# Optimization experiments

Hardware: AMD Instinct MI355X
Metric: run time of the kernel (lower is better)

## Reference

```python
import jax, jax.numpy as jnp
import numpy as np

D = 1024
H = 16
EPS = 1e-5


def setup_inputs() -> dict:
    key = jax.random.key(0)
    ks = jax.random.split(key, 6)
    B, T, d = 4, 2048, D
    s = 0.02
    return {
        "x": jax.random.normal(ks[0], (B, T, d), jnp.float32),
        "w_attn": jax.random.normal(ks[1], (d, 3 * d), jnp.float32) * s,
        "w_o": jax.random.normal(ks[2], (d, d), jnp.float32) * s,
        "ln1_g": jnp.ones((d,), jnp.float32),
        "ln1_b": jnp.zeros((d,), jnp.float32),
        "ln2_g": jnp.ones((d,), jnp.float32),
        "ln2_b": jnp.zeros((d,), jnp.float32),
        "w_fc": jax.random.normal(ks[3], (d, 4 * d), jnp.float32) * s,
        "b_fc": jnp.zeros((4 * d,), jnp.float32),
        "w_proj": jax.random.normal(ks[4], (4 * d, d), jnp.float32) * s,
        "b_proj": jnp.zeros((d,), jnp.float32),
    }


def _layernorm(x, g, b):
    mu = jnp.mean(x, axis=-1, keepdims=True)
    var = jnp.mean(jnp.square(x - mu), axis=-1, keepdims=True)
    return (x - mu) * jax.lax.rsqrt(var + EPS) * g + b


def _attention(x, w_attn, w_o):
    B, T, d = x.shape
    hd = d // H
    qkv = x @ w_attn  # [B,T,3d]
    q, k, v = jnp.split(qkv, 3, axis=-1)
    q = q.reshape(B, T, H, hd).transpose(0, 2, 1, 3)  # [B,H,T,hd]
    k = k.reshape(B, T, H, hd).transpose(0, 2, 1, 3)
    v = v.reshape(B, T, H, hd).transpose(0, 2, 1, 3)
    att = jnp.einsum("bhqd,bhkd->bhqk", q, k) * (1.0 / np.sqrt(hd))
    mask = jnp.tril(jnp.ones((T, T), bool))
    att = jnp.where(mask, att, jnp.float32(-jnp.inf))
    att = jax.nn.softmax(att, axis=-1)
    y = jnp.einsum("bhqk,bhkd->bhqd", att, v)
    y = y.transpose(0, 2, 1, 3).reshape(B, T, d)
    return y @ w_o


def reference(x, w_attn, w_o, ln1_g, ln1_b, ln2_g, ln2_b, w_fc, b_fc, w_proj, b_proj):
    x = x + _attention(_layernorm(x, ln1_g, ln1_b), w_attn, w_o)
    h = _layernorm(x, ln2_g, ln2_b)
    h = jax.nn.gelu(h @ w_fc + b_fc, approximate=True)
    return x + h @ w_proj + b_proj
```

## Files before the change

### kernel.cpp

```cpp
#include <hip/hip_runtime.h>
#include <math.h>

#define D_MODEL 1024
#define NHEAD   16
#define HDIM    64
#define SEQ     2048
#define BATCH   4
#define NROWS   (BATCH*SEQ)

using bf16x8 = __attribute__((ext_vector_type(8))) short;
using bf16x4 = __attribute__((ext_vector_type(4))) short;
using f32x4  = __attribute__((ext_vector_type(4))) float;

__device__ __forceinline__ unsigned short f2bf(float f) {
    unsigned u = __float_as_uint(f);
    u += 0x7fffu + ((u >> 16) & 1u);
    return (unsigned short)(u >> 16);
}
__device__ __forceinline__ float bf2f(unsigned short h) {
    unsigned u = ((unsigned)h) << 16;
    return __uint_as_float(u);
}

#define ASYNC_COPY16(g, l) \
    __builtin_amdgcn_global_load_lds((__attribute__((address_space(1))) const void*)(g), \
                                     (__attribute__((address_space(3))) void*)(l), 16, 0, 0)

__global__ __launch_bounds__(256) void ln_kernel(const float* __restrict__ x,
                                                 const float* __restrict__ g,
                                                 const float* __restrict__ b,
                                                 unsigned short* __restrict__ out) {
    const int row = blockIdx.x;
    const int tid = threadIdx.x;
    const float4* x4 = (const float4*)(x + (size_t)row * D_MODEL);
    float4 v = x4[tid];
    float s  = v.x + v.y + v.z + v.w;
    float sq = v.x*v.x + v.y*v.y + v.z*v.z + v.w*v.w;
    #pragma unroll
    for (int off = 32; off >= 1; off >>= 1) {
        s  += __shfl_down(s,  off, 64);
        sq += __shfl_down(sq, off, 64);
    }
    __shared__ float rs[4], rq[4];
    const int wave = tid >> 6;
    if ((tid & 63) == 0) { rs[wave] = s; rq[wave] = sq; }
    __syncthreads();
    const float tot  = rs[0] + rs[1] + rs[2] + rs[3];
    const float totq = rq[0] + rq[1] + rq[2] + rq[3];
    const float mu   = tot * (1.0f / D_MODEL);
    const float var  = totq * (1.0f / D_MODEL) - mu * mu;
    const float rstd = rsqrtf(var + 1e-5f);
    const float4 gv = ((const float4*)g)[tid];
    const float4 bv = ((const float4*)b)[tid];
    unsigned short* o = out + (size_t)row * D_MODEL + tid * 4;
    o[0] = f2bf((v.x - mu) * rstd * gv.x + bv.x);
    o[1] = f2bf((v.y - mu) * rstd * gv.y + bv.y);
    o[2] = f2bf((v.z - mu) * rstd * gv.z + bv.z);
    o[3] = f2bf((v.w - mu) * rstd * gv.w + bv.w);
}

__global__ __launch_bounds__(256) void wt_kernel(const float* __restrict__ w,
                                                 unsigned short* __restrict__ wt,
                                                 int K, int N) {
    __shared__ float tile[32][33];
    const int n0 = blockIdx.x * 32, k0 = blockIdx.y * 32;
    const int tx = threadIdx.x & 31, ty = threadIdx.x >> 5;
    #pragma unroll
    for (int j = 0; j < 4; ++j)
        tile[ty + j * 8][tx] = w[(size_t)(k0 + ty + j * 8) * N + n0 + tx];
    __syncthreads();
    #pragma unroll
    for (int j = 0; j < 4; ++j)
        wt[(size_t)(n0 + ty + j * 8) * K + k0 + tx] = f2bf(tile[tx][ty + j * 8]);
}

template<int MODE>
__global__ __launch_bounds__(256, 2) void gemm2p(const unsigned short* __restrict__ A,
                                                 const unsigned short* __restrict__ Bt,
                                                 const float* __restrict__ bias,
                                                 unsigned short* __restrict__ outp,
                                                 unsigned short* __restrict__ vt_out,
                                                 int M, int N, int K, int Kslice) {
    __shared__ __align__(16) unsigned short As[2][256 * 32];
    __shared__ __align__(16) unsigned short Bs[2][128 * 32];

    const int tid  = threadIdx.x;
    const int lane = tid & 63;
    const int wave = __builtin_amdgcn_readfirstlane(tid >> 6);
    const int quad = lane >> 4, l16 = lane & 15;
    const int wm = wave >> 1, wn = wave & 1;
    const int m0 = blockIdx.x * 256, n0 = blockIdx.y * 128;

    int kbeg = 0, klen = K;
    if (MODE == 1) {
        kbeg = blockIdx.z * Kslice;
        klen = (blockIdx.z == (int)gridDim.z - 1) ? (K - kbeg) : Kslice;
    }
    const int nt = klen >> 5;

    const int rA = tid >> 2;
    const int cs = ((tid & 3) ^ ((rA >> 1) & 3)) * 8;
    const unsigned short* Ag[4];
    const unsigned short* Bg[2];
    #pragma unroll
    for (int g = 0; g < 4; ++g)
        Ag[g] = A + (size_t)(m0 + g * 64 + rA) * K + cs + kbeg;
    #pragma unroll
    for (int g = 0; g < 2; ++g)
        Bg[g] = Bt + (size_t)(n0 + g * 64 + rA) * K + cs + kbeg;

#define STAGE(tt, bb) do { const int ko_ = (tt) * 32;                          \
        ASYNC_COPY16(Ag[0] + ko_, &As[bb][           tid * 8]);                \
        ASYNC_COPY16(Ag[1] + ko_, &As[bb][ 2048 +    tid * 8]);                \
        ASYNC_COPY16(Ag[2] + ko_, &As[bb][ 4096 +    tid * 8]);                \
        ASYNC_COPY16(Ag[3] + ko_, &As[bb][ 6144 +    tid * 8]);                \
        ASYNC_COPY16(Bg[0] + ko_, &Bs[bb][           tid * 8]);                \
        ASYNC_COPY16(Bg[1] + ko_, &Bs[bb][ 2048 +    tid * 8]);                \
    } while (0)

    const int rc = (quad ^ ((l16 >> 1) & 3)) * 8;

    f32x4 acc[8][4] = {};

    STAGE(0, 0); STAGE(1, 1);
    asm volatile("s_waitcnt vmcnt(6)" ::: "memory");
    __builtin_amdgcn_s_barrier();

    for (int t = 0; t < nt; ++t) {
        const int bb = t & 1;
        bf16x8 a[8], b[4];
        #pragma unroll
        for (int i = 0; i < 8; ++i)
            a[i] = *(const bf16x8*)&As[bb][(wm * 128 + i * 16 + l16) * 32 + rc];
        #pragma unroll
        for (int j = 0; j < 4; ++j)
            b[j] = *(const bf16x8*)&Bs[bb][(wn * 64 + j * 16 + l16) * 32 + rc];
        __builtin_amdgcn_s_barrier();
        asm volatile("s_waitcnt lgkmcnt(0)" ::: "memory");
        __builtin_amdgcn_s_setprio(1);
        #pragma unroll
        for (int i = 0; i < 8; ++i) {
            acc[i][0] = __builtin_amdgcn_mfma_f32_16x16x32_bf16(a[i], b[0], acc[i][0], 0, 0, 0);
            acc[i][1] = __builtin_amdgcn_mfma_f32_16x16x32_bf16(a[i], b[1], acc[i][1], 0, 0, 0);
        }
        __builtin_amdgcn_s_setprio(0);
        __builtin_amdgcn_s_barrier();
        if (t + 2 < nt) STAGE(t + 2, bb);
        __builtin_amdgcn_s_setprio(1);
        #pragma unroll
        for (int i = 0; i < 8; ++i) {
            acc[i][2] = __builtin_amdgcn_mfma_f32_16x16x32_bf16(a[i], b[2], acc[i][2], 0, 0, 0);
            acc[i][3] = __builtin_amdgcn_mfma_f32_16x16x32_bf16(a[i], b[3], acc[i][3], 0, 0, 0);
        }
        __builtin_amdgcn_s_setprio(0);
        if (t + 2 < nt) asm volatile("s_waitcnt vmcnt(6)" ::: "memory");
        else            asm volatile("s_waitcnt vmcnt(0)" ::: "memory");
        __builtin_amdgcn_s_barrier();
    }
#undef STAGE

    if (MODE == 0) {
        #pragma unroll
        for (int i = 0; i < 8; ++i)
          #pragma unroll
          for (int j = 0; j < 4; ++j)
            #pragma unroll
            for (int r = 0; r < 4; ++r) {
                const int row = m0 + wm * 128 + i * 16 + quad * 4 + r;
                const int col = n0 + wn * 64 + j * 16 + l16;
                float v = acc[i][j][r] + bias[col];
                const float u = 0.7978845608028654f * (v + 0.044715f * v * v * v);
                const float e = __expf(2.0f * u);
                v = 0.5f * v * (2.0f - 2.0f / (e + 1.0f));
                outp[(size_t)row * N + col] = f2bf(v);
            }
    } else if (MODE == 1) {
        unsigned short* outb = outp + (size_t)blockIdx.z * M * N;
        #pragma unroll
        for (int i = 0; i < 8; ++i)
          #pragma unroll
          for (int j = 0; j < 4; ++j)
            #pragma unroll
            for (int r = 0; r < 4; ++r) {
                const int row = m0 + wm * 128 + i * 16 + quad * 4 + r;
                const int col = n0 + wn * 64 + j * 16 + l16;
                outb[(size_t)row * N + col] = f2bf(acc[i][j][r]);
            }
    } else {
        if (n0 < 2048) {
            const float sc = (n0 < 1024) ? 0.125f : 1.0f;
            #pragma unroll
            for (int i = 0; i < 8; ++i)
              #pragma unroll
              for (int j = 0; j < 4; ++j)
                #pragma unroll
                for (int r = 0; r < 4; ++r) {
                    const int row = m0 + wm * 128 + i * 16 + quad * 4 + r;
                    const int col = n0 + wn * 64 + j * 16 + l16;
                    outp[(size_t)row * 2048 + col] = f2bf(acc[i][j][r] * sc);
                }
        } else {
            #pragma unroll
            for (int i = 0; i < 8; ++i)
              #pragma unroll
              for (int j = 0; j < 4; ++j) {
                    const int dv  = n0 - 2048 + wn * 64 + j * 16 + l16;
                    const int tok = m0 + wm * 128 + i * 16 + quad * 4;
                    ushort4 pk;
                    pk.x = f2bf(acc[i][j][0]); pk.y = f2bf(acc[i][j][1]);
                    pk.z = f2bf(acc[i][j][2]); pk.w = f2bf(acc[i][j][3]);
                    *(ushort4*)(vt_out + (size_t)dv * NROWS + tok) = pk;
                }
        }
    }
}

template<int NP>
__global__ __launch_bounds__(256) void reduce_wo_ln2(const float* __restrict__ x,
                                                     const unsigned short* __restrict__ pw,
                                                     const float* __restrict__ g,
                                                     const float* __restrict__ bb,
                                                     float* __restrict__ out,
                                                     unsigned short* __restrict__ lnout) {
    const int row = blockIdx.x;
    const int tid = threadIdx.x;
    const size_t base = (size_t)row * D_MODEL + tid * 4;
    const size_t stride = (size_t)NROWS * D_MODEL;
    float4 v = *(const float4*)(x + base);
    #pragma unroll
    for (int z = 0; z < NP; ++z) {
        ushort4 a = *(const ushort4*)(pw + z * stride + base);
        v.x += bf2f(a.x); v.y += bf2f(a.y); v.z += bf2f(a.z); v.w += bf2f(a.w);
    }
    *(float4*)(out + base) = v;

    float s  = v.x + v.y + v.z + v.w;
    float sq = v.x*v.x + v.y*v.y + v.z*v.z + v.w*v.w;
    #pragma unroll
    for (int off = 32; off >= 1; off >>= 1) {
        s  += __shfl_down(s,  off, 64);
        sq += __shfl_down(sq, off, 64);
    }
    __shared__ float rs[4], rq[4];
    const int wave = tid >> 6;
    if ((tid & 63) == 0) { rs[wave] = s; rq[wave] = sq; }
    __syncthreads();
    const float tot  = rs[0] + rs[1] + rs[2] + rs[3];
    const float totq = rq[0] + rq[1] + rq[2] + rq[3];
    const float mu   = tot * (1.0f / D_MODEL);
    const float var  = totq * (1.0f / D_MODEL) - mu * mu;
    const float rstd = rsqrtf(var + 1e-5f);
    const float4 gv = ((const float4*)g)[tid];
    const float4 bv = ((const float4*)bb)[tid];
    unsigned short* o = lnout + (size_t)row * D_MODEL + tid * 4;
    o[0] = f2bf((v.x - mu) * rstd * gv.x + bv.x);
    o[1] = f2bf((v.y - mu) * rstd * gv.y + bv.y);
    o[2] = f2bf((v.z - mu) * rstd * gv.z + bv.z);
    o[3] = f2bf((v.w - mu) * rstd * gv.w + bv.w);
}

template<int NP>
__global__ __launch_bounds__(256) void reduce_kernel(float* __restrict__ out,
                                                     const unsigned short* __restrict__ pp,
                                                     const float* __restrict__ bias) {
    const int row = blockIdx.x;
    const int c0 = threadIdx.x * 4;
    const size_t base = (size_t)row * D_MODEL + c0;
    const size_t stride = (size_t)NROWS * D_MODEL;
    float4 o = *(float4*)(out + base);
    const float4 bs = *(const float4*)(bias + c0);
    o.x += bs.x; o.y += bs.y; o.z += bs.z; o.w += bs.w;
    #pragma unroll
    for (int z = 0; z < NP; ++z) {
        ushort4 a = *(const ushort4*)(pp + z * stride + base);
        o.x += bf2f(a.x); o.y += bf2f(a.y); o.z += bf2f(a.z); o.w += bf2f(a.w);
    }
    *(float4*)(out + base) = o;
}

__global__ __launch_bounds__(256) void attn_kernel(const unsigned short* __restrict__ qk,
                                                   const unsigned short* __restrict__ VT,
                                                   unsigned short* __restrict__ y) {
    __shared__ __align__(16) unsigned short Qs[128 * 64];
    __shared__ __align__(16) unsigned short Ks[64 * 64];
    __shared__ __align__(16) unsigned short Vs[80 * 64];
    __shared__ __align__(16) unsigned short Ps[128 * 68];

    const int tid  = threadIdx.x;
    const int lane = tid & 63, w = tid >> 6;
    const int quad = lane >> 4, l16 = lane & 15;
    const int s7   = l16 & 7;
    const int pc0  = (quad ^ s7) * 8;
    const int pc1  = ((quad + 4) ^ s7) * 8;
    const int srow = tid >> 3, sp = tid & 7;

    const int pairidx = blockIdx.x;
    const int bh = blockIdx.y;
    const int b = bh >> 4, h = bh & 15;
    const size_t rowbase = (size_t)b * SEQ;
    const unsigned short* Qbase = qk + h * 64;
    const unsigned short* Kbase = qk + 1024 + h * 64;
    const unsigned short* Vbase = VT + (size_t)(h * 64) * NROWS + b * SEQ;

    #pragma unroll
    for (int e = 0; e < 4; ++e) {
        const int off = tid * 4 + e;
        Vs[4096 + off] = (off < 64) ? (unsigned short)0x3F80 : (unsigned short)0;
    }

    for (int phase = 0; phase < 2; ++phase) {
        const int Q = phase ? pairidx : (15 - pairidx);
        const int nkt = 2 * Q + 2;
        const int qg0 = Q * 128;

        #pragma unroll
        for (int i = 0; i < 4; ++i) {
            const int row = i * 32 + srow;
            const int c = sp ^ (row & 7);
            ASYNC_COPY16(Qbase + (rowbase + qg0 + row) * 2048 + c * 8,
                         (char*)Qs + i * 4096 + tid * 16);
        }
        __syncthreads();

        bf16x8 aq[2][2];
        #pragma unroll
        for (int sub = 0; sub < 2; ++sub) {
            const int qrow = sub * 64 + w * 16 + l16;
            aq[sub][0] = *(const bf16x8*)&Qs[qrow * 64 + pc0];
            aq[sub][1] = *(const bf16x8*)&Qs[qrow * 64 + pc1];
        }

        f32x4 o[2][5] = {};

        for (int kt = 0; kt < nkt; ++kt) {
            #pragma unroll
            for (int i = 0; i < 2; ++i) {
                const int row = i * 32 + srow;
                const int c = sp ^ (row & 7);
                ASYNC_COPY16(Kbase + (rowbase + kt * 64 + row) * 2048 + c * 8,
                             (char*)Ks + i * 4096 + tid * 16);
                ASYNC_COPY16(Vbase + (size_t)row * NROWS + kt * 64 + c * 8,
                             (char*)Vs + i * 4096 + tid * 16);
            }
            __syncthreads();

            bf16x8 bk[4][2];
            #pragma unroll
            for (int cb = 0; cb < 4; ++cb) {
                const int krow = cb * 16 + l16;
                bk[cb][0] = *(const bf16x8*)&Ks[krow * 64 + pc0];
                bk[cb][1] = *(const bf16x8*)&Ks[krow * 64 + pc1];
            }

            #pragma unroll
            for (int sub = 0; sub < 2; ++sub) {
                if (kt > 2 * Q + sub) continue;
                f32x4 s[4] = {};
                #pragma unroll
                for (int cb = 0; cb < 4; ++cb) {
                    s[cb] = __builtin_amdgcn_mfma_f32_16x16x32_bf16(aq[sub][0], bk[cb][0], s[cb], 0, 0, 0);
                    s[cb] = __builtin_amdgcn_mfma_f32_16x16x32_bf16(aq[sub][1], bk[cb][1], s[cb], 0, 0, 0);
                }
                const int prow0 = sub * 64 + w * 16 + quad * 4;
                if (kt == 2 * Q + sub) {
                    const int qg = qg0 + prow0;
                    const int kg = kt * 64 + l16;
                    #pragma unroll
                    for (int cb = 0; cb < 4; ++cb)
                        #pragma unroll
                        for (int r = 0; r < 4; ++r) {
                            const float e = __expf(s[cb][r]);
                            const float pv = (kg + cb * 16 > qg + r) ? 0.0f : e;
                            Ps[(prow0 + r) * 68 + cb * 16 + l16] = f2bf(pv);
                        }
                } else {
                    #pragma unroll
                    for (int cb = 0; cb < 4; ++cb)
                        #pragma unroll
                        for (int r = 0; r < 4; ++r)
                            Ps[(prow0 + r) * 68 + cb * 16 + l16] = f2bf(__expf(s[cb][r]));
                }
            }
            __syncthreads();

            bf16x8 bv[5][2];
            #pragma unroll
            for (int db = 0; db < 5; ++db) {
                const int vrow = db * 16 + l16;
                bv[db][0] = *(const bf16x8*)&Vs[vrow * 64 + pc0];
                bv[db][1] = *(const bf16x8*)&Vs[vrow * 64 + pc1];
            }
            #pragma unroll
            for (int sub = 0; sub < 2; ++sub) {
                if (kt > 2 * Q + sub) continue;
                const unsigned short* pb = &Ps[(sub * 64 + w * 16 + l16) * 68];
                bf16x8 ap0, ap1;
                *(bf16x4*)&ap0       = *(const bf16x4*)(pb + quad * 8);
                *((bf16x4*)&ap0 + 1) = *(const bf16x4*)(pb + quad * 8 + 4);
                *(bf16x4*)&ap1       = *(const bf16x4*)(pb + 32 + quad * 8);
                *((bf16x4*)&ap1 + 1) = *(const bf16x4*)(pb + 32 + quad * 8 + 4);
                #pragma unroll
                for (int db = 0; db < 5; ++db) {
                    o[sub][db] = __builtin_amdgcn_mfma_f32_16x16x32_bf16(ap0, bv[db][0], o[sub][db], 0, 0, 0);
                    o[sub][db] = __builtin_amdgcn_mfma_f32_16x16x32_bf16(ap1, bv[db][1], o[sub][db], 0, 0, 0);
                }
            }
            __syncthreads();
        }

        #pragma unroll
        for (int sub = 0; sub < 2; ++sub)
            #pragma unroll
            for (int r = 0; r < 4; ++r) {
                const float lsum = __shfl(o[sub][4][r], lane & 48);
                const float rinv = 1.0f / lsum;
                const int trow = qg0 + sub * 64 + w * 16 + quad * 4 + r;
                unsigned short* yp = y + (rowbase + trow) * (size_t)D_MODEL + h * 64 + l16;
                #pragma unroll
                for (int db = 0; db < 4; ++db)
                    yp[db * 16] = f2bf(o[sub][db][r] * rinv);
            }
    }
}

extern "C" void kernel_launch(void* const* d_in, const int* in_sizes, int n_in,
                              void* d_out, int out_size, void* d_ws, size_t ws_size,
                              hipStream_t stream) {
    (void)in_sizes; (void)n_in; (void)out_size; (void)ws_size;
    const float* x      = (const float*)d_in[0];
    const float* w_attn = (const float*)d_in[1];
    const float* w_o    = (const float*)d_in[2];
    const float* ln1_g  = (const float*)d_in[3];
    const float* ln1_b  = (const float*)d_in[4];
    const float* ln2_g  = (const float*)d_in[5];
    const float* ln2_b  = (const float*)d_in[6];
    const float* w_fc   = (const float*)d_in[7];
    const float* b_fc   = (const float*)d_in[8];
    const float* w_proj = (const float*)d_in[9];
    const float* b_proj = (const float*)d_in[10];
    float* out = (float*)d_out;

    char* ws = (char*)d_ws;
    const size_t MiB = 1048576;
    unsigned short* ln_buf  = (unsigned short*)ws;
    unsigned short* qkbuf   = (unsigned short*)(ws + 16 * MiB);
    unsigned short* VTbuf   = (unsigned short*)(ws + 48 * MiB);
    unsigned short* wt_attn = (unsigned short*)(ws + 64 * MiB);
    unsigned short* hbuf    = (unsigned short*)(ws + 64 * MiB);
    unsigned short* wt_o    = (unsigned short*)(ws + 126 * MiB);
    unsigned short* pw      = (unsigned short*)(ws + 16 * MiB);
    unsigned short* wt_fc   = (unsigned short*)(ws + 48 * MiB);
    unsigned short* wt_proj = (unsigned short*)(ws + 56 * MiB);
    unsigned short* pp      = (unsigned short*)ws;

    wt_kernel<<<dim3(3072 / 32, 1024 / 32), 256, 0, stream>>>(w_attn, wt_attn, 1024, 3072);
    wt_kernel<<<dim3(1024 / 32, 1024 / 32), 256, 0, stream>>>(w_o, wt_o, 1024, 1024);

    ln_kernel<<<NROWS, 256, 0, stream>>>(x, ln1_g, ln1_b, ln_buf);

    gemm2p<2><<<dim3(NROWS / 256, 3072 / 128), 256, 0, stream>>>(
        ln_buf, wt_attn, nullptr, qkbuf, VTbuf, NROWS, 3072, 1024, 0);

    attn_kernel<<<dim3(8, BATCH * NHEAD), 256, 0, stream>>>(qkbuf, VTbuf, ln_buf);

    gemm2p<1><<<dim3(NROWS / 256, 1024 / 128, 2), 256, 0, stream>>>(
        ln_buf, wt_o, nullptr, pw, nullptr, NROWS, 1024, 1024, 512);
    reduce_wo_ln2<2><<<NROWS, 256, 0, stream>>>(x, pw, ln2_g, ln2_b, out, ln_buf);

    wt_kernel<<<dim3(4096 / 32, 1024 / 32), 256, 0, stream>>>(w_fc, wt_fc, 1024, 4096);
    wt_kernel<<<dim3(1024 / 32, 4096 / 32), 256, 0, stream>>>(w_proj, wt_proj, 4096, 1024);

    gemm2p<0><<<dim3(NROWS / 256, 4096 / 128), 256, 0, stream>>>(
        ln_buf, wt_fc, b_fc, hbuf, nullptr, NROWS, 4096, 1024, 0);

    gemm2p<1><<<dim3(NROWS / 256, 1024 / 128, 2), 256, 0, stream>>>(
        hbuf, wt_proj, nullptr, pp, nullptr, NROWS, 1024, 4096, 2048);
    reduce_kernel<2><<<NROWS, 256, 0, stream>>>(out, pp, b_proj);
}
```

Before: 496.6 us.

## Single-buffer GEMM with BK=64 and double-buffer K/V tiles in attention

The GEMM drops its double-buffered BK=32 async pipeline, with its fine-grained barriers and priority hints, in favour of a single-buffered BK=64 tile loaded and then computed between two __syncthreads. The attention kernel gains double-buffered K/V shared tiles, prefetching the next tile while the current one is processed. The ones-column used for row sums moves to its own buffer, and one barrier is replaced by an lgkmcnt wait. The GEMM change gives up load/compute overlap in exchange for fewer barriers, while the attention change aims to hide K/V load latency at the cost of more shared memory.

```diff
diff --git a/kernel.cpp b/kernel.cpp
--- a/kernel.cpp
+++ b/kernel.cpp
@@ -75,14 +75,14 @@
 }
 
 template<int MODE>
-__global__ __launch_bounds__(256, 2) void gemm2p(const unsigned short* __restrict__ A,
-                                                 const unsigned short* __restrict__ Bt,
-                                                 const float* __restrict__ bias,
-                                                 unsigned short* __restrict__ outp,
-                                                 unsigned short* __restrict__ vt_out,
-                                                 int M, int N, int K, int Kslice) {
-    __shared__ __align__(16) unsigned short As[2][256 * 32];
-    __shared__ __align__(16) unsigned short Bs[2][128 * 32];
+__global__ __launch_bounds__(256, 2) void gemm_big(const unsigned short* __restrict__ A,
+                                                   const unsigned short* __restrict__ Bt,
+                                                   const float* __restrict__ bias,
+                                                   unsigned short* __restrict__ outp,
+                                                   unsigned short* __restrict__ vt_out,
+                                                   int M, int N, int K, int Kslice) {
+    __shared__ __align__(16) unsigned short As[256 * 64];
+    __shared__ __align__(16) unsigned short Bs[128 * 64];
 
     const int tid  = threadIdx.x;
     const int lane = tid & 63;
@@ -96,68 +96,50 @@
         kbeg = blockIdx.z * Kslice;
         klen = (blockIdx.z == (int)gridDim.z - 1) ? (K - kbeg) : Kslice;
     }
-    const int nt = klen >> 5;
-
-    const int rA = tid >> 2;
-    const int cs = ((tid & 3) ^ ((rA >> 1) & 3)) * 8;
-    const unsigned short* Ag[4];
-    const unsigned short* Bg[2];
-    #pragma unroll
-    for (int g = 0; g < 4; ++g)
-        Ag[g] = A + (size_t)(m0 + g * 64 + rA) * K + cs + kbeg;
-    #pragma unroll
-    for (int g = 0; g < 2; ++g)
-        Bg[g] = Bt + (size_t)(n0 + g * 64 + rA) * K + cs + kbeg;
-
-#define STAGE(tt, bb) do { const int ko_ = (tt) * 32;                          \
-        ASYNC_COPY16(Ag[0] + ko_, &As[bb][           tid * 8]);                \
-        ASYNC_COPY16(Ag[1] + ko_, &As[bb][ 2048 +    tid * 8]);                \
-        ASYNC_COPY16(Ag[2] + ko_, &As[bb][ 4096 +    tid * 8]);                \
-        ASYNC_COPY16(Ag[3] + ko_, &As[bb][ 6144 +    tid * 8]);                \
-        ASYNC_COPY16(Bg[0] + ko_, &Bs[bb][           tid * 8]);                \
-        ASYNC_COPY16(Bg[1] + ko_, &Bs[bb][ 2048 +    tid * 8]);                \
-    } while (0)
-
-    const int rc = (quad ^ ((l16 >> 1) & 3)) * 8;
 
     f32x4 acc[8][4] = {};
 
-    STAGE(0, 0); STAGE(1, 1);
-    asm volatile("s_waitcnt vmcnt(6)" ::: "memory");
-    __builtin_amdgcn_s_barrier();
-
-    for (int t = 0; t < nt; ++t) {
-        const int bb = t & 1;
-        bf16x8 a[8], b[4];
+    const int rr  = tid >> 3;
+    const int p   = tid & 7;
+    const int gch = (p ^ (rr & 7)) * 8;
+
+    const unsigned short* Ag[8];
+    const unsigned short* Bg[4];
+    #pragma unroll
+    for (int i = 0; i < 8; ++i)
+        Ag[i] = A + (size_t)(m0 + i * 32 + rr) * K + gch + kbeg;
+    #pragma unroll
+    for (int i = 0; i < 4; ++i)
+        Bg[i] = Bt + (size_t)(n0 + i * 32 + rr) * K + gch + kbeg;
+
+    const int pc = (quad ^ (l16 & 7)) * 8;
+
+    for (int kb = 0; kb < klen; kb += 64) {
         #pragma unroll
         for (int i = 0; i < 8; ++i)
-            a[i] = *(const bf16x8*)&As[bb][(wm * 128 + i * 16 + l16) * 32 + rc];
-        #pragma unroll
-        for (int j = 0; j < 4; ++j)
-            b[j] = *(const bf16x8*)&Bs[bb][(wn * 64 + j * 16 + l16) * 32 + rc];
-        __builtin_amdgcn_s_barrier();
-        asm volatile("s_waitcnt lgkmcnt(0)" ::: "memory");
-        __builtin_amdgcn_s_setprio(1);
-        #pragma unroll
-        for (int i = 0; i < 8; ++i) {
-            acc[i][0] = __builtin_amdgcn_mfma_f32_16x16x32_bf16(a[i], b[0], acc[i][0], 0, 0, 0);
-            acc[i][1] = __builtin_amdgcn_mfma_f32_16x16x32_bf16(a[i], b[1], acc[i][1], 0, 0, 0);
+            ASYNC_COPY16(Ag[i] + kb, As + i * 2048 + tid * 8);
+        #pragma unroll
+        for (int i = 0; i < 4; ++i)
+            ASYNC_COPY16(Bg[i] + kb, Bs + i * 2048 + tid * 8);
+        __syncthreads();
+
+        #pragma unroll
+        for (int half = 0; half < 2; ++half) {
+            const int off = half ? (pc ^ 32) : pc;
+            bf16x8 b[4];
+            #pragma unroll
+            for (int j = 0; j < 4; ++j)
+                b[j] = *(const bf16x8*)&Bs[(wn * 64 + j * 16 + l16) * 64 + off];
+            #pragma unroll
+            for (int i = 0; i < 8; ++i) {
+                bf16x8 a = *(const bf16x8*)&As[(wm * 128 + i * 16 + l16) * 64 + off];
+                #pragma unroll
+                for (int j = 0; j < 4; ++j)
+                    acc[i][j] = __builtin_amdgcn_mfma_f32_16x16x32_bf16(a, b[j], acc[i][j], 0, 0, 0);
+            }
         }
-        __builtin_amdgcn_s_setprio(0);
-        __builtin_amdgcn_s_barrier();
-        if (t + 2 < nt) STAGE(t + 2, bb);
-        __builtin_amdgcn_s_setprio(1);
-        #pragma unroll
-        for (int i = 0; i < 8; ++i) {
-            acc[i][2] = __builtin_amdgcn_mfma_f32_16x16x32_bf16(a[i], b[2], acc[i][2], 0, 0, 0);
-            acc[i][3] = __builtin_amdgcn_mfma_f32_16x16x32_bf16(a[i], b[3], acc[i][3], 0, 0, 0);
-        }
-        __builtin_amdgcn_s_setprio(0);
-        if (t + 2 < nt) asm volatile("s_waitcnt vmcnt(6)" ::: "memory");
-        else            asm volatile("s_waitcnt vmcnt(0)" ::: "memory");
-        __builtin_amdgcn_s_barrier();
-    }
-#undef STAGE
+        __syncthreads();
+    }
 
     if (MODE == 0) {
         #pragma unroll
@@ -282,8 +264,9 @@
                                                    const unsigned short* __restrict__ VT,
                                                    unsigned short* __restrict__ y) {
     __shared__ __align__(16) unsigned short Qs[128 * 64];
-    __shared__ __align__(16) unsigned short Ks[64 * 64];
-    __shared__ __align__(16) unsigned short Vs[80 * 64];
+    __shared__ __align__(16) unsigned short Ks[2][64 * 64];
+    __shared__ __align__(16) unsigned short Vs[2][64 * 64];
+    __shared__ __align__(16) unsigned short Ones[16 * 64];
     __shared__ __align__(16) unsigned short Ps[128 * 68];
 
     const int tid  = threadIdx.x;
@@ -293,6 +276,7 @@
     const int pc0  = (quad ^ s7) * 8;
     const int pc1  = ((quad + 4) ^ s7) * 8;
     const int srow = tid >> 3, sp = tid & 7;
+    const int sc   = sp ^ (srow & 7);
 
     const int pairidx = blockIdx.x;
     const int bh = blockIdx.y;
@@ -302,10 +286,15 @@
     const unsigned short* Kbase = qk + 1024 + h * 64;
     const unsigned short* Vbase = VT + (size_t)(h * 64) * NROWS + b * SEQ;
 
+    const unsigned short* Kg0 = Kbase + (rowbase + srow) * 2048 + sc * 8;
+    const unsigned short* Kg1 = Kg0 + (size_t)32 * 2048;
+    const unsigned short* Vg0 = Vbase + (size_t)srow * NROWS + sc * 8;
+    const unsigned short* Vg1 = Vg0 + (size_t)32 * NROWS;
+
     #pragma unroll
     for (int e = 0; e < 4; ++e) {
         const int off = tid * 4 + e;
-        Vs[4096 + off] = (off < 64) ? (unsigned short)0x3F80 : (unsigned short)0;
+        Ones[off] = (off < 64) ? (unsigned short)0x3F80 : (unsigned short)0;
     }
 
     for (int phase = 0; phase < 2; ++phase) {
@@ -314,12 +303,13 @@
         const int qg0 = Q * 128;
 
         #pragma unroll
-        for (int i = 0; i < 4; ++i) {
-            const int row = i * 32 + srow;
-            const int c = sp ^ (row & 7);
-            ASYNC_COPY16(Qbase + (rowbase + qg0 + row) * 2048 + c * 8,
+        for (int i = 0; i < 4; ++i)
+            ASYNC_COPY16(Qbase + (rowbase + qg0 + i * 32 + srow) * 2048 + sc * 8,
                          (char*)Qs + i * 4096 + tid * 16);
-        }
+        ASYNC_COPY16(Kg0, (char*)&Ks[0][0] + tid * 16);
+        ASYNC_COPY16(Kg1, (char*)&Ks[0][0] + 4096 + tid * 16);
+        ASYNC_COPY16(Vg0, (char*)&Vs[0][0] + tid * 16);
+        ASYNC_COPY16(Vg1, (char*)&Vs[0][0] + 4096 + tid * 16);
         __syncthreads();
 
         bf16x8 aq[2][2];
@@ -333,23 +323,22 @@
         f32x4 o[2][5] = {};
 
         for (int kt = 0; kt < nkt; ++kt) {
-            #pragma unroll
-            for (int i = 0; i < 2; ++i) {
-                const int row = i * 32 + srow;
-                const int c = sp ^ (row & 7);
-                ASYNC_COPY16(Kbase + (rowbase + kt * 64 + row) * 2048 + c * 8,
-                             (char*)Ks + i * 4096 + tid * 16);
-                ASYNC_COPY16(Vbase + (size_t)row * NROWS + kt * 64 + c * 8,
-                             (char*)Vs + i * 4096 + tid * 16);
-            }
-            __syncthreads();
+            const int buf = kt & 1;
+            if (kt + 1 < nkt) {
+                const size_t koK = (size_t)(kt + 1) * 64 * 2048;
+                const size_t koV = (size_t)(kt + 1) * 64;
+                ASYNC_COPY16(Kg0 + koK, (char*)&Ks[buf ^ 1][0] + tid * 16);
+                ASYNC_COPY16(Kg1 + koK, (char*)&Ks[buf ^ 1][0] + 4096 + tid * 16);
+                ASYNC_COPY16(Vg0 + koV, (char*)&Vs[buf ^ 1][0] + tid * 16);
+                ASYNC_COPY16(Vg1 + koV, (char*)&Vs[buf ^ 1][0] + 4096 + tid * 16);
+            }
 
             bf16x8 bk[4][2];
             #pragma unroll
             for (int cb = 0; cb < 4; ++cb) {
                 const int krow = cb * 16 + l16;
-                bk[cb][0] = *(const bf16x8*)&Ks[krow * 64 + pc0];
-                bk[cb][1] = *(const bf16x8*)&Ks[krow * 64 + pc1];
+                bk[cb][0] = *(const bf16x8*)&Ks[buf][krow * 64 + pc0];
+                bk[cb][1] = *(const bf16x8*)&Ks[buf][krow * 64 + pc1];
             }
 
             #pragma unroll
@@ -381,15 +370,18 @@
                             Ps[(prow0 + r) * 68 + cb * 16 + l16] = f2bf(__expf(s[cb][r]));
                 }
             }
-            __syncthreads();
+            asm volatile("s_waitcnt lgkmcnt(0)" ::: "memory");
 
             bf16x8 bv[5][2];
             #pragma unroll
-            for (int db = 0; db < 5; ++db) {
+            for (int db = 0; db < 4; ++db) {
                 const int vrow = db * 16 + l16;
-                bv[db][0] = *(const bf16x8*)&Vs[vrow * 64 + pc0];
-                bv[db][1] = *(const bf16x8*)&Vs[vrow * 64 + pc1];
-            }
+                bv[db][0] = *(const bf16x8*)&Vs[buf][vrow * 64 + pc0];
+                bv[db][1] = *(const bf16x8*)&Vs[buf][vrow * 64 + pc1];
+            }
+            bv[4][0] = *(const bf16x8*)&Ones[l16 * 64 + pc0];
+            bv[4][1] = *(const bf16x8*)&Ones[l16 * 64 + pc1];
+
             #pragma unroll
             for (int sub = 0; sub < 2; ++sub) {
                 if (kt > 2 * Q + sub) continue;
@@ -405,6 +397,7 @@
                     o[sub][db] = __builtin_amdgcn_mfma_f32_16x16x32_bf16(ap1, bv[db][1], o[sub][db], 0, 0, 0);
                 }
             }
+            asm volatile("s_waitcnt vmcnt(0)" ::: "memory");
             __syncthreads();
         }
 
@@ -458,22 +451,22 @@
 
     ln_kernel<<<NROWS, 256, 0, stream>>>(x, ln1_g, ln1_b, ln_buf);
 
-    gemm2p<2><<<dim3(NROWS / 256, 3072 / 128), 256, 0, stream>>>(
+    gemm_big<2><<<dim3(NROWS / 256, 3072 / 128), 256, 0, stream>>>(
         ln_buf, wt_attn, nullptr, qkbuf, VTbuf, NROWS, 3072, 1024, 0);
 
     attn_kernel<<<dim3(8, BATCH * NHEAD), 256, 0, stream>>>(qkbuf, VTbuf, ln_buf);
 
-    gemm2p<1><<<dim3(NROWS / 256, 1024 / 128, 2), 256, 0, stream>>>(
+    gemm_big<1><<<dim3(NROWS / 256, 1024 / 128, 2), 256, 0, stream>>>(
         ln_buf, wt_o, nullptr, pw, nullptr, NROWS, 1024, 1024, 512);
     reduce_wo_ln2<2><<<NROWS, 256, 0, stream>>>(x, pw, ln2_g, ln2_b, out, ln_buf);
 
     wt_kernel<<<dim3(4096 / 32, 1024 / 32), 256, 0, stream>>>(w_fc, wt_fc, 1024, 4096);
     wt_kernel<<<dim3(1024 / 32, 4096 / 32), 256, 0, stream>>>(w_proj, wt_proj, 4096, 1024);
 
-    gemm2p<0><<<dim3(NROWS / 256, 4096 / 128), 256, 0, stream>>>(
+    gemm_big<0><<<dim3(NROWS / 256, 4096 / 128), 256, 0, stream>>>(
         ln_buf, wt_fc, b_fc, hbuf, nullptr, NROWS, 4096, 1024, 0);
 
-    gemm2p<1><<<dim3(NROWS / 256, 1024 / 128, 2), 256, 0, stream>>>(
+    gemm_big<1><<<dim3(NROWS / 256, 1024 / 128, 2), 256, 0, stream>>>(
         hbuf, wt_proj, nullptr, pp, nullptr, NROWS, 1024, 4096, 2048);
     reduce_kernel<2><<<NROWS, 256, 0, stream>>>(out, pp, b_proj);
 }
```

Result: faster. 478.2 us (-3.7%).
